# Performance work log

Measured on AMD Instinct MI355X. Metric: run time of the kernel, lower is better.

The kernel has to match this reference:

```python
import jax, jax.numpy as jnp
import numpy as np

# Dimensions: B jets, P max particles, C coords, F features, K neighbors,
# H hidden units, O MLP output dim. Edge feature dim E = 2*(C+F).
B, P, C, F, K, H, O = 256, 128, 2, 7, 16, 128, 256
E = 2 * (C + F)
BIG = 1e9  # distance assigned to invalid (padded) neighbors


def setup_inputs() -> dict:
    key = jax.random.key(0)
    k1, k2, k3, k4 = jax.random.split(key, 4)
    raw = jax.random.normal(k1, (B, P, C + F), dtype=jnp.float32)
    # per-jet particle counts in [K+2, P]; padding is contiguous at the end
    lengths = jax.random.randint(k2, (B,), K + 2, P + 1)
    mask = (jnp.arange(P)[None, :] < lengths[:, None]).astype(jnp.float32)  # [B,P]
    # zero out padded rows and append mask as the last column (as the layer expects)
    x = jnp.concatenate([raw * mask[..., None], mask[..., None]], axis=-1)  # [B,P,C+F+1]
    W1 = jax.random.normal(k3, (E, H), dtype=jnp.float32) * (1.0 / np.sqrt(E))
    b1 = jnp.zeros((H,), dtype=jnp.float32)
    W2 = jax.random.normal(k4, (H, O), dtype=jnp.float32) * (1.0 / np.sqrt(H))
    b2 = jnp.zeros((O,), dtype=jnp.float32)
    return {"x": x, "W1": W1, "b1": b1, "W2": W2, "b2": b2}


def reference(x, W1, b1, W2, b2):
    coords = x[..., :C]          # [B,P,C]
    feats = x[..., C:-1]         # [B,P,F]
    mask = x[..., -1]            # [B,P] 1=real particle, 0=padding
    valid = mask > 0

    # --- kNN on coordinates (masked, vectorized over jets) ---
    diff = coords[:, :, None, :] - coords[:, None, :, :]      # [B,P,P,C]
    # squared distance: same ordering as tf.norm, avoids sqrt-at-zero issues
    dist2 = jnp.sum(diff * diff, axis=-1)                      # [B,P,P]
    dist2 = jnp.where(valid[:, None, :], dist2, BIG)           # mask padded neighbors
    _, idx = jax.lax.top_k(-dist2, K + 1)                      # [B,P,K+1]
    idx = idx[..., 1:]                                         # drop self -> [B,P,K]

    # --- gather neighbor coords/features ---
    idx_flat = idx.reshape(B, P * K)
    nbr_c = jnp.take_along_axis(coords, idx_flat[..., None], axis=1).reshape(B, P, K, C)
    nbr_f = jnp.take_along_axis(feats, idx_flat[..., None], axis=1).reshape(B, P, K, F)
    ctr_c = jnp.broadcast_to(coords[:, :, None, :], (B, P, K, C))
    ctr_f = jnp.broadcast_to(feats[:, :, None, :], (B, P, K, F))

    # edge features: [coord_i, feat_i, coord_j - coord_i, feat_j - feat_i]
    edge = jnp.concatenate([ctr_c, ctr_f, nbr_c - ctr_c, nbr_f - ctr_f], axis=-1)  # [B,P,K,E]

    # --- MLP + mean aggregation over neighbors ---
    h = jax.nn.relu(edge @ W1 + b1)   # [B,P,K,H]
    h = jax.nn.relu(h @ W2 + b2)      # [B,P,K,O]
    avg = jnp.mean(h, axis=2)         # [B,P,O]

    # append mask column; zero out padded particles (matches _fix_number_of_particles)
    out = jnp.concatenate([avg, jnp.ones((B, P, 1), avg.dtype)], axis=-1) * mask[..., None]
    return out
```

## Files before the change

kernel.cpp:

```cpp
#include <hip/hip_runtime.h>

#define BB 256
#define PP 128
#define KK 16
#define HH 128
#define OO 256
#define EE 18
#define XCH 10
#define BIGD 1000000000.0f
#define GPT 8
#define NBLK ((BB * PP) / GPT)

typedef __bf16 bf16x8 __attribute__((ext_vector_type(8)));
typedef __bf16 bf16x4 __attribute__((ext_vector_type(4)));
typedef float  f32x4  __attribute__((ext_vector_type(4)));
typedef unsigned long long ull;

__global__ __launch_bounds__(256) void pack_w_kernel(const float* __restrict__ W1,
                                                     const float* __restrict__ W2,
                                                     __bf16* __restrict__ W2p,
                                                     __bf16* __restrict__ W1p) {
    const int t = blockIdx.x * 256 + threadIdx.x;
    if (t < 32768) {
        const int j  = t & 7;
        const int l  = (t >> 3) & 63;
        const int ks = (t >> 9) & 3;
        const int ct = t >> 11;
        const int row = ks * 32 + ((l >> 4) * 8) + j;
        const int col = ct * 16 + (l & 15);
        W2p[t] = (__bf16)W2[row * OO + col];
    } else {
        const int t2 = t - 32768;
        const int j  = t2 & 7;
        const int l  = (t2 >> 3) & 63;
        const int nt = t2 >> 9;
        const int k  = ((l >> 4) * 8) + j;
        const int n  = nt * 16 + (l & 15);
        W1p[t2] = (k < EE) ? (__bf16)W1[k * HH + n] : (__bf16)0.0f;
    }
}

__global__ __launch_bounds__(256, 4) void mlp_kernel(const float* __restrict__ x,
                                                     const __bf16* __restrict__ W1p,
                                                     const float* __restrict__ b1,
                                                     const __bf16* __restrict__ W2p,
                                                     const float* __restrict__ b2,
                                                     float* __restrict__ out) {
    __shared__ __bf16 sh1A[4 * GPT * 64 * 8];
    __shared__ int    sknn[GPT][KK];

    const int tid = threadIdx.x;
    const int lane = tid & 63;
    const int w = tid >> 6;
    const int quad = lane >> 4;
    const int lcol = lane & 15;

    const int pbase = blockIdx.x * GPT;
    const int bidx = pbase >> 7;
    const int i0 = pbase & (PP - 1);
    const float* xb = x + (size_t)bidx * PP * XCH;
    float* outrow = out + (size_t)pbase * (OO + 1);

    const float mph = xb[(i0 + (lane & 7)) * XCH + (XCH - 1)];
    if (__all(mph == 0.0f)) {
        for (int o = tid; o < GPT * (OO + 1); o += 256) outrow[o] = 0.0f;
        return;
    }

    const int j0 = lane, j1 = lane + 64;
    const float2 c0 = *(const float2*)(xb + j0 * XCH);
    const float  m0 = xb[j0 * XCH + (XCH - 1)];
    const float2 c1 = *(const float2*)(xb + j1 * XCH);
    const float  m1 = xb[j1 * XCH + (XCH - 1)];

    const int gA = w * 2, gB = w * 2 + 1;
    const int iA = i0 + gA, iB = i0 + gB;
    const float2 ccA = *(const float2*)(xb + iA * XCH);
    const float  mA  = xb[iA * XCH + (XCH - 1)];
    const float2 ccB = *(const float2*)(xb + iB * XCH);
    const float  mB  = xb[iB * XCH + (XCH - 1)];

    bf16x8 wf[8];
#pragma unroll
    for (int nt = 0; nt < 8; ++nt)
        wf[nt] = *(const bf16x8*)&W1p[(size_t)((nt * 64 + lane) * 8)];

    unsigned db0[2], db1[2];
    {
        float dx, dy, d;
        dx = ccA.x - c0.x; dy = ccA.y - c0.y;
        d = __fadd_rn(__fmul_rn(dx, dx), __fmul_rn(dy, dy));
        if (m0 <= 0.0f || j0 == iA) d = BIGD;
        db0[0] = __float_as_uint(d);
        dx = ccA.x - c1.x; dy = ccA.y - c1.y;
        d = __fadd_rn(__fmul_rn(dx, dx), __fmul_rn(dy, dy));
        if (m1 <= 0.0f || j1 == iA) d = BIGD;
        db1[0] = __float_as_uint(d);
        dx = ccB.x - c0.x; dy = ccB.y - c0.y;
        d = __fadd_rn(__fmul_rn(dx, dx), __fmul_rn(dy, dy));
        if (m0 <= 0.0f || j0 == iB) d = BIGD;
        db0[1] = __float_as_uint(d);
        dx = ccB.x - c1.x; dy = ccB.y - c1.y;
        d = __fadd_rn(__fmul_rn(dx, dx), __fmul_rn(dy, dy));
        if (m1 <= 0.0f || j1 == iB) d = BIGD;
        db1[1] = __float_as_uint(d);
    }

    const bool act[2] = {mA != 0.0f, mB != 0.0f};
    ull A0[2], A1[2], W0[2], W1g[2];
    int need[2], asz[2];
#pragma unroll
    for (int p = 0; p < 2; ++p) {
        A0[p] = ~0ull; A1[p] = ~0ull; W0[p] = 0ull; W1g[p] = 0ull;
        need[p] = act[p] ? KK : 0;
        asz[p] = 128;
    }

#pragma unroll 1
    for (int t = 14; t >= 0; --t) {
#pragma unroll
        for (int p = 0; p < 2; ++p) {
            if (need[p]) {
                const unsigned dg0 = (db0[p] >> (2 * t + 1)) & 3u;
                const unsigned dg1 = (db1[p] >> (2 * t + 1)) & 3u;
                const ull p0_0  = __ballot(dg0 == 0u);
                const ull p1_0  = __ballot(dg1 == 0u);
                const ull p0_01 = __ballot(dg0 <= 1u);
                const ull p1_01 = __ballot(dg1 <= 1u);
                const ull p0_02 = __ballot(dg0 <= 2u);
                const ull p1_02 = __ballot(dg1 <= 2u);
                const ull z0_0  = A0[p] & p0_0,  z1_0  = A1[p] & p1_0;
                const ull z0_01 = A0[p] & p0_01, z1_01 = A1[p] & p1_01;
                const ull z0_02 = A0[p] & p0_02, z1_02 = A1[p] & p1_02;
                const int c0c = __popcll(z0_0)  + __popcll(z1_0);
                const int c01 = __popcll(z0_01) + __popcll(z1_01);
                const int c02 = __popcll(z0_02) + __popcll(z1_02);
                if (c0c >= need[p]) {
                    A0[p] = z0_0; A1[p] = z1_0; asz[p] = c0c;
                } else if (c01 >= need[p]) {
                    W0[p] |= z0_0; W1g[p] |= z1_0; need[p] -= c0c;
                    A0[p] = z0_01 & ~p0_0; A1[p] = z1_01 & ~p1_0; asz[p] = c01 - c0c;
                } else if (c02 >= need[p]) {
                    W0[p] |= z0_01; W1g[p] |= z1_01; need[p] -= c01;
                    A0[p] = z0_02 & ~p0_01; A1[p] = z1_02 & ~p1_01; asz[p] = c02 - c01;
                } else {
                    W0[p] |= z0_02; W1g[p] |= z1_02; need[p] -= c02;
                    A0[p] &= ~p0_02; A1[p] &= ~p1_02; asz[p] -= c02;
                }
                if (asz[p] == need[p]) {
                    W0[p] |= A0[p]; W1g[p] |= A1[p];
                    A0[p] = A1[p] = 0ull; need[p] = 0;
                }
            }
        }
        if (!(need[0] | need[1])) break;
    }
#pragma unroll
    for (int p = 0; p < 2; ++p) {
        auto stepP = [&](ull q0, ull q1) {
            const ull z0 = A0[p] & q0;
            const ull z1 = A1[p] & q1;
            const int c = __popcll(z0) + __popcll(z1);
            if (c == need[p]) { W0[p] |= z0; W1g[p] |= z1; A0[p] = A1[p] = 0ull; need[p] = 0; }
            else if (c > need[p]) { A0[p] = z0; A1[p] = z1; asz[p] = c; }
            else { W0[p] |= z0; W1g[p] |= z1; need[p] -= c; A0[p] &= ~z0; A1[p] &= ~z1; asz[p] -= c; }
        };
        if (need[p]) {
            const ull q0 = __ballot((db0[p] & 1u) == 0u);
            const ull q1 = __ballot((db1[p] & 1u) == 0u);
            stepP(q0, q1);
        }
        if (need[p]) stepP(~0ull, 0ull);
        {
            const ull M5 = 0x00000000FFFFFFFFull;
            const ull M4 = 0x0000FFFF0000FFFFull;
            const ull M3 = 0x00FF00FF00FF00FFull;
            const ull M2 = 0x0F0F0F0F0F0F0F0Full;
            const ull M1 = 0x3333333333333333ull;
            const ull M0 = 0x5555555555555555ull;
            if (need[p]) stepP(M5, M5);
            if (need[p]) stepP(M4, M4);
            if (need[p]) stepP(M3, M3);
            if (need[p]) stepP(M2, M2);
            if (need[p]) stepP(M1, M1);
            if (need[p]) stepP(M0, M0);
        }
        W0[p] |= A0[p]; W1g[p] |= A1[p];

        const int g = w * 2 + p;
        if (act[p]) {
            unsigned int mb0 = __builtin_amdgcn_mbcnt_lo((unsigned)(W0[p] & 0xffffffffull), 0u);
            mb0 = __builtin_amdgcn_mbcnt_hi((unsigned)(W0[p] >> 32), mb0);
            unsigned int mb1 = __builtin_amdgcn_mbcnt_lo((unsigned)(W1g[p] & 0xffffffffull), 0u);
            mb1 = __builtin_amdgcn_mbcnt_hi((unsigned)(W1g[p] >> 32), mb1);
            const int base1 = __popcll(W0[p]);
            if ((W0[p] >> lane) & 1ull) sknn[g][mb0] = j0;
            if ((W1g[p] >> lane) & 1ull) sknn[g][base1 + mb1] = j1;
        } else {
            if (lane < KK) sknn[g][lane] = 0;
        }
    }

    const f32x4 z4 = {0.0f, 0.0f, 0.0f, 0.0f};
#pragma unroll
    for (int p = 0; p < 2; ++p) {
        const int g = w * 2 + p;
        const int ip = i0 + g;
        const int jn = sknn[g][lcol];
        const float* ciP = xb + ip * XCH;
        const float* cjP = xb + jn * XCH;
        const float2 a01 = *(const float2*)(ciP + 0);
        const float2 a23 = *(const float2*)(ciP + 2);
        const float2 a45 = *(const float2*)(ciP + 4);
        const float2 a67 = *(const float2*)(ciP + 6);
        const float  a8  = ciP[8];
        const float2 n01 = *(const float2*)(cjP + 0);
        const float2 n23 = *(const float2*)(cjP + 2);
        const float2 n45 = *(const float2*)(cjP + 4);
        const float2 n67 = *(const float2*)(cjP + 6);
        const float  n8  = cjP[8];

        float v[8];
#pragma unroll
        for (int e = 0; e < 8; ++e) v[e] = 0.0f;
        if (quad == 0) {
            v[0] = a01.x; v[1] = a01.y; v[2] = a23.x; v[3] = a23.y;
            v[4] = a45.x; v[5] = a45.y; v[6] = a67.x; v[7] = a67.y;
        } else if (quad == 1) {
            v[0] = a8;
            v[1] = n01.x - a01.x; v[2] = n01.y - a01.y;
            v[3] = n23.x - a23.x; v[4] = n23.y - a23.y;
            v[5] = n45.x - a45.x; v[6] = n45.y - a45.y;
            v[7] = n67.x - a67.x;
        } else if (quad == 2) {
            v[0] = n67.y - a67.y;
            v[1] = n8 - a8;
        }

        bf16x8 ef;
#pragma unroll
        for (int e = 0; e < 8; ++e) ef[e] = (__bf16)v[e];

        f32x4 hh[8];
#pragma unroll
        for (int nt = 0; nt < 8; ++nt)
            hh[nt] = __builtin_amdgcn_mfma_f32_16x16x32_bf16(wf[nt], ef, z4, 0, 0, 0);

#pragma unroll
        for (int nt = 0; nt < 8; ++nt) {
            const int ks = nt >> 1;
            const int lp = (((nt * 2 + (quad >> 1)) & 3) << 4) | lcol;
            const f32x4 b1v = *(const f32x4*)&b1[nt * 16 + quad * 4];
            bf16x4 hv;
#pragma unroll
            for (int r = 0; r < 4; ++r)
                hv[r] = (__bf16)fmaxf(hh[nt][r] + b1v[r], 0.0f);
            *(bf16x4*)&sh1A[((ks * GPT + g) * 64 + lp) * 8 + (quad & 1) * 4] = hv;
        }
    }
    __syncthreads();

#pragma unroll
    for (int gg = 0; gg < 2; ++gg) {
#pragma unroll
        for (int ch = 0; ch < 2; ++ch) {
            f32x4 acc[4][2];
#pragma unroll
            for (int gi = 0; gi < 4; ++gi) { acc[gi][0] = z4; acc[gi][1] = z4; }

#pragma unroll
            for (int ks = 0; ks < 4; ++ks) {
                bf16x8 af[4], bfr[2];
#pragma unroll
                for (int gi = 0; gi < 4; ++gi)
                    af[gi] = *(const bf16x8*)&sh1A[((ks * GPT + gg * 4 + gi) * 64 + lane) * 8];
#pragma unroll
                for (int c = 0; c < 2; ++c)
                    bfr[c] = *(const bf16x8*)&W2p[(size_t)((((w * 4 + ch * 2 + c) * 4 + ks) * 64 + lane) * 8)];
#pragma unroll
                for (int gi = 0; gi < 4; ++gi)
#pragma unroll
                    for (int c = 0; c < 2; ++c)
                        acc[gi][c] = __builtin_amdgcn_mfma_f32_16x16x32_bf16(
                            af[gi], bfr[c], acc[gi][c], 0, 0, 0);
            }

#pragma unroll
            for (int c = 0; c < 2; ++c) {
                const int col = w * 64 + (ch * 2 + c) * 16 + lcol;
                const float bc = b2[col];
                float val = 0.0f;
#pragma unroll
                for (int gi = 0; gi < 4; ++gi) {
                    float s = 0.0f;
#pragma unroll
                    for (int r = 0; r < 4; ++r) s += fmaxf(acc[gi][c][r] + bc, 0.0f);
                    s += __shfl_xor(s, 16, 64);
                    s += __shfl_xor(s, 32, 64);
                    if (quad == gi) val = s;
                }
                const float mp = xb[(i0 + gg * 4 + quad) * XCH + (XCH - 1)];
                outrow[(size_t)(gg * 4 + quad) * (OO + 1) + col] = val * (mp * (1.0f / KK));
            }
        }
    }
    if (tid < GPT)
        outrow[(size_t)tid * (OO + 1) + OO] = xb[(i0 + tid) * XCH + (XCH - 1)];
}

extern "C" void kernel_launch(void* const* d_in, const int* in_sizes, int n_in,
                              void* d_out, int out_size, void* d_ws, size_t ws_size,
                              hipStream_t stream) {
    const float* x  = (const float*)d_in[0];
    const float* W1 = (const float*)d_in[1];
    const float* b1 = (const float*)d_in[2];
    const float* W2 = (const float*)d_in[3];
    const float* b2 = (const float*)d_in[4];
    float* out = (float*)d_out;

    __bf16* W2p = (__bf16*)d_ws;
    __bf16* W1p = (__bf16*)((char*)d_ws + 65536);

    pack_w_kernel<<<144, 256, 0, stream>>>(W1, W2, W2p, W1p);

    mlp_kernel<<<NBLK, 256, 0, stream>>>(x, W1p, b1, W2p, b2, out);
}
```

Before: 126.6 us.

## Replace ballot radix-select kNN with packed-key bitonic sort and merge

Swaps the ballot/popcount radix-select top-K search for a wavefront-wide bitonic sort over 64-bit keys that pack the distance bits with the particle index. Each lane's two keys are sorted in registers and across lanes with shuffles, and three lower-half merge steps shrink the candidate set to the 16 nearest. The neighbour indices then go straight to lanes by shuffle, so the shared-memory kNN table and its writes are removed. This removes the data-dependent loop and branching, but every jet now pays a fixed and fairly long chain of 64-bit shuffles. Inactive particles now get real neighbour indices instead of zeros; their outputs are presumably still masked later.

```diff
diff --git a/kernel.cpp b/kernel.cpp
--- a/kernel.cpp
+++ b/kernel.cpp
@@ -15,6 +15,12 @@
 typedef __bf16 bf16x4 __attribute__((ext_vector_type(4)));
 typedef float  f32x4  __attribute__((ext_vector_type(4)));
 typedef unsigned long long ull;
+
+__device__ __forceinline__ ull shfl_xor64(ull v, int m) {
+    const int lo = __shfl_xor((int)(unsigned)v, m, 64);
+    const int hi = __shfl_xor((int)(unsigned)(v >> 32), m, 64);
+    return ((ull)(unsigned)hi << 32) | (unsigned)lo;
+}
 
 __global__ __launch_bounds__(256) void pack_w_kernel(const float* __restrict__ W1,
                                                      const float* __restrict__ W2,
@@ -47,7 +53,6 @@
                                                      const float* __restrict__ b2,
                                                      float* __restrict__ out) {
     __shared__ __bf16 sh1A[4 * GPT * 64 * 8];
-    __shared__ int    sknn[GPT][KK];
 
     const int tid = threadIdx.x;
     const int lane = tid & 63;
@@ -73,140 +78,107 @@
     const float2 c1 = *(const float2*)(xb + j1 * XCH);
     const float  m1 = xb[j1 * XCH + (XCH - 1)];
 
-    const int gA = w * 2, gB = w * 2 + 1;
-    const int iA = i0 + gA, iB = i0 + gB;
+    const int iA = i0 + w * 2, iB = i0 + w * 2 + 1;
     const float2 ccA = *(const float2*)(xb + iA * XCH);
-    const float  mA  = xb[iA * XCH + (XCH - 1)];
     const float2 ccB = *(const float2*)(xb + iB * XCH);
-    const float  mB  = xb[iB * XCH + (XCH - 1)];
 
     bf16x8 wf[8];
 #pragma unroll
     for (int nt = 0; nt < 8; ++nt)
         wf[nt] = *(const bf16x8*)&W1p[(size_t)((nt * 64 + lane) * 8)];
 
-    unsigned db0[2], db1[2];
+    ull k0[2], k1[2];
     {
         float dx, dy, d;
         dx = ccA.x - c0.x; dy = ccA.y - c0.y;
         d = __fadd_rn(__fmul_rn(dx, dx), __fmul_rn(dy, dy));
         if (m0 <= 0.0f || j0 == iA) d = BIGD;
-        db0[0] = __float_as_uint(d);
+        k0[0] = ((ull)__float_as_uint(d) << 7) | (unsigned)j0;
         dx = ccA.x - c1.x; dy = ccA.y - c1.y;
         d = __fadd_rn(__fmul_rn(dx, dx), __fmul_rn(dy, dy));
         if (m1 <= 0.0f || j1 == iA) d = BIGD;
-        db1[0] = __float_as_uint(d);
+        k1[0] = ((ull)__float_as_uint(d) << 7) | (unsigned)j1;
         dx = ccB.x - c0.x; dy = ccB.y - c0.y;
         d = __fadd_rn(__fmul_rn(dx, dx), __fmul_rn(dy, dy));
         if (m0 <= 0.0f || j0 == iB) d = BIGD;
-        db0[1] = __float_as_uint(d);
+        k0[1] = ((ull)__float_as_uint(d) << 7) | (unsigned)j0;
         dx = ccB.x - c1.x; dy = ccB.y - c1.y;
         d = __fadd_rn(__fmul_rn(dx, dx), __fmul_rn(dy, dy));
         if (m1 <= 0.0f || j1 == iB) d = BIGD;
-        db1[1] = __float_as_uint(d);
-    }
-
-    const bool act[2] = {mA != 0.0f, mB != 0.0f};
-    ull A0[2], A1[2], W0[2], W1g[2];
-    int need[2], asz[2];
-#pragma unroll
-    for (int p = 0; p < 2; ++p) {
-        A0[p] = ~0ull; A1[p] = ~0ull; W0[p] = 0ull; W1g[p] = 0ull;
-        need[p] = act[p] ? KK : 0;
-        asz[p] = 128;
-    }
-
-#pragma unroll 1
-    for (int t = 14; t >= 0; --t) {
-#pragma unroll
-        for (int p = 0; p < 2; ++p) {
-            if (need[p]) {
-                const unsigned dg0 = (db0[p] >> (2 * t + 1)) & 3u;
-                const unsigned dg1 = (db1[p] >> (2 * t + 1)) & 3u;
-                const ull p0_0  = __ballot(dg0 == 0u);
-                const ull p1_0  = __ballot(dg1 == 0u);
-                const ull p0_01 = __ballot(dg0 <= 1u);
-                const ull p1_01 = __ballot(dg1 <= 1u);
-                const ull p0_02 = __ballot(dg0 <= 2u);
-                const ull p1_02 = __ballot(dg1 <= 2u);
-                const ull z0_0  = A0[p] & p0_0,  z1_0  = A1[p] & p1_0;
-                const ull z0_01 = A0[p] & p0_01, z1_01 = A1[p] & p1_01;
-                const ull z0_02 = A0[p] & p0_02, z1_02 = A1[p] & p1_02;
-                const int c0c = __popcll(z0_0)  + __popcll(z1_0);
-                const int c01 = __popcll(z0_01) + __popcll(z1_01);
-                const int c02 = __popcll(z0_02) + __popcll(z1_02);
-                if (c0c >= need[p]) {
-                    A0[p] = z0_0; A1[p] = z1_0; asz[p] = c0c;
-                } else if (c01 >= need[p]) {
-                    W0[p] |= z0_0; W1g[p] |= z1_0; need[p] -= c0c;
-                    A0[p] = z0_01 & ~p0_0; A1[p] = z1_01 & ~p1_0; asz[p] = c01 - c0c;
-                } else if (c02 >= need[p]) {
-                    W0[p] |= z0_01; W1g[p] |= z1_01; need[p] -= c01;
-                    A0[p] = z0_02 & ~p0_01; A1[p] = z1_02 & ~p1_01; asz[p] = c02 - c01;
-                } else {
-                    W0[p] |= z0_02; W1g[p] |= z1_02; need[p] -= c02;
-                    A0[p] &= ~p0_02; A1[p] &= ~p1_02; asz[p] -= c02;
-                }
-                if (asz[p] == need[p]) {
-                    W0[p] |= A0[p]; W1g[p] |= A1[p];
-                    A0[p] = A1[p] = 0ull; need[p] = 0;
-                }
-            }
-        }
-        if (!(need[0] | need[1])) break;
-    }
-#pragma unroll
-    for (int p = 0; p < 2; ++p) {
-        auto stepP = [&](ull q0, ull q1) {
-            const ull z0 = A0[p] & q0;
-            const ull z1 = A1[p] & q1;
-            const int c = __popcll(z0) + __popcll(z1);
-            if (c == need[p]) { W0[p] |= z0; W1g[p] |= z1; A0[p] = A1[p] = 0ull; need[p] = 0; }
-            else if (c > need[p]) { A0[p] = z0; A1[p] = z1; asz[p] = c; }
-            else { W0[p] |= z0; W1g[p] |= z1; need[p] -= c; A0[p] &= ~z0; A1[p] &= ~z1; asz[p] -= c; }
-        };
-        if (need[p]) {
-            const ull q0 = __ballot((db0[p] & 1u) == 0u);
-            const ull q1 = __ballot((db1[p] & 1u) == 0u);
-            stepP(q0, q1);
-        }
-        if (need[p]) stepP(~0ull, 0ull);
-        {
-            const ull M5 = 0x00000000FFFFFFFFull;
-            const ull M4 = 0x0000FFFF0000FFFFull;
-            const ull M3 = 0x00FF00FF00FF00FFull;
-            const ull M2 = 0x0F0F0F0F0F0F0F0Full;
-            const ull M1 = 0x3333333333333333ull;
-            const ull M0 = 0x5555555555555555ull;
-            if (need[p]) stepP(M5, M5);
-            if (need[p]) stepP(M4, M4);
-            if (need[p]) stepP(M3, M3);
-            if (need[p]) stepP(M2, M2);
-            if (need[p]) stepP(M1, M1);
-            if (need[p]) stepP(M0, M0);
-        }
-        W0[p] |= A0[p]; W1g[p] |= A1[p];
-
-        const int g = w * 2 + p;
-        if (act[p]) {
-            unsigned int mb0 = __builtin_amdgcn_mbcnt_lo((unsigned)(W0[p] & 0xffffffffull), 0u);
-            mb0 = __builtin_amdgcn_mbcnt_hi((unsigned)(W0[p] >> 32), mb0);
-            unsigned int mb1 = __builtin_amdgcn_mbcnt_lo((unsigned)(W1g[p] & 0xffffffffull), 0u);
-            mb1 = __builtin_amdgcn_mbcnt_hi((unsigned)(W1g[p] >> 32), mb1);
-            const int base1 = __popcll(W0[p]);
-            if ((W0[p] >> lane) & 1ull) sknn[g][mb0] = j0;
-            if ((W1g[p] >> lane) & 1ull) sknn[g][base1 + mb1] = j1;
-        } else {
-            if (lane < KK) sknn[g][lane] = 0;
-        }
-    }
+        k1[1] = ((ull)__float_as_uint(d) << 7) | (unsigned)j1;
+    }
+
+    auto ce_x = [&](ull &k, int sm, int upm) {
+        const ull pk = shfl_xor64(k, sm);
+        const bool wmin = (((upm == 0) || ((lane & upm) == 0)) == ((lane & sm) == 0));
+        const ull mn = (k < pk) ? k : pk;
+        const ull mx = (k < pk) ? pk : k;
+        k = wmin ? mn : mx;
+    };
+    auto ce_s = [&](ull &a, ull &b, int upm) {
+        const bool up = (upm == 0) || ((lane & upm) == 0);
+        const ull mn = (a < b) ? a : b;
+        const ull mx = (a < b) ? b : a;
+        a = up ? mn : mx;
+        b = up ? mx : mn;
+    };
+
+#pragma unroll
+    for (int pt = 0; pt < 2; ++pt) ce_s(k0[pt], k1[pt], 1);
+#pragma unroll
+    for (int pt = 0; pt < 2; ++pt) { ce_x(k0[pt], 1, 2); ce_x(k1[pt], 1, 2); }
+#pragma unroll
+    for (int pt = 0; pt < 2; ++pt) ce_s(k0[pt], k1[pt], 2);
+#pragma unroll
+    for (int pt = 0; pt < 2; ++pt) { ce_x(k0[pt], 2, 4); ce_x(k1[pt], 2, 4); }
+#pragma unroll
+    for (int pt = 0; pt < 2; ++pt) { ce_x(k0[pt], 1, 4); ce_x(k1[pt], 1, 4); }
+#pragma unroll
+    for (int pt = 0; pt < 2; ++pt) ce_s(k0[pt], k1[pt], 4);
+#pragma unroll
+    for (int pt = 0; pt < 2; ++pt) { ce_x(k0[pt], 4, 0); ce_x(k1[pt], 4, 0); }
+#pragma unroll
+    for (int pt = 0; pt < 2; ++pt) { ce_x(k0[pt], 2, 0); ce_x(k1[pt], 2, 0); }
+#pragma unroll
+    for (int pt = 0; pt < 2; ++pt) { ce_x(k0[pt], 1, 0); ce_x(k1[pt], 1, 0); }
+#pragma unroll
+    for (int pt = 0; pt < 2; ++pt) ce_s(k0[pt], k1[pt], 0);
+
+    auto merge_lo = [&](ull &a, ull &b, int revm, bool resort) {
+        const ull ra = shfl_xor64(a, revm);
+        const ull rb = shfl_xor64(b, revm);
+        const ull na = (a < rb) ? a : rb;
+        const ull nb = (b < ra) ? b : ra;
+        a = na; b = nb;
+        if (resort) {
+            ce_x(a, 4, 0); ce_x(b, 4, 0);
+            ce_x(a, 2, 0); ce_x(b, 2, 0);
+            ce_x(a, 1, 0); ce_x(b, 1, 0);
+            ce_s(a, b, 0);
+        }
+    };
+#pragma unroll
+    for (int pt = 0; pt < 2; ++pt) merge_lo(k0[pt], k1[pt], 15, true);
+#pragma unroll
+    for (int pt = 0; pt < 2; ++pt) merge_lo(k0[pt], k1[pt], 23, true);
+#pragma unroll
+    for (int pt = 0; pt < 2; ++pt) merge_lo(k0[pt], k1[pt], 39, false);
+
+    const int srcl = (lane & 15) >> 1;
+    const unsigned pkA = (unsigned)(k0[0] & 127) | ((unsigned)(k1[0] & 127) << 8);
+    const unsigned pkB = (unsigned)(k0[1] & 127) | ((unsigned)(k1[1] & 127) << 8);
+    const unsigned gA = (unsigned)__shfl((int)pkA, srcl, 64);
+    const unsigned gB = (unsigned)__shfl((int)pkB, srcl, 64);
+    int jn2[2];
+    jn2[0] = (int)(((lane & 1) ? (gA >> 8) : gA) & 127u);
+    jn2[1] = (int)(((lane & 1) ? (gB >> 8) : gB) & 127u);
 
     const f32x4 z4 = {0.0f, 0.0f, 0.0f, 0.0f};
 #pragma unroll
     for (int p = 0; p < 2; ++p) {
         const int g = w * 2 + p;
         const int ip = i0 + g;
-        const int jn = sknn[g][lcol];
+        const int jn = jn2[p];
         const float* ciP = xb + ip * XCH;
         const float* cjP = xb + jn * XCH;
         const float2 a01 = *(const float2*)(ciP + 0);
```

Result: slower. 133.2 us (+5.2%).
